# Kernel tuning notes

Measured on AMD Instinct MI355X. Metric: run time of the kernel, lower is better.

## Reference

```python
import jax, jax.numpy as jnp
import numpy as np

B, S, D, H = 2, 2048, 1024, 16
DK = D // H  # 64


def setup_inputs() -> dict:
    key = jax.random.key(0)
    ks = jax.random.split(key, 4)
    scale = 1.0 / np.sqrt(D)
    return {
        "q_input": jax.random.normal(ks[0], (B, S, D), dtype=jnp.float32),
        "W_q": jax.random.normal(ks[1], (D, D), dtype=jnp.float32) * scale,
        "b_q": jnp.zeros((D,), dtype=jnp.float32),
        "W_k": jax.random.normal(ks[2], (D, D), dtype=jnp.float32) * scale,
        "b_k": jnp.zeros((D,), dtype=jnp.float32),
        "W_v": jax.random.normal(ks[3], (D, D), dtype=jnp.float32) * scale,
        "b_v": jnp.zeros((D,), dtype=jnp.float32),
    }


def reference(q_input, W_q, b_q, W_k, b_k, W_v, b_v):
    # Self-attention: k_input and v_input default to q_input in the torch module.
    # nn.Linear computes x @ W.T + b
    q = q_input @ W_q.T + b_q
    k = q_input @ W_k.T + b_k
    v = q_input @ W_v.T + b_v

    # [B,S,D] -> [B,H,S,DK]
    def split_heads(x):
        return x.reshape(B, S, H, DK).transpose(0, 2, 1, 3)

    qh, kh, vh = split_heads(q), split_heads(k), split_heads(v)

    # scores [B,H,S,S]; causal mask added BEFORE scaling (as in source; -inf invariant)
    scores = jnp.einsum("bhqd,bhkd->bhqk", qh, kh)
    causal = jnp.tril(jnp.ones((S, S), dtype=bool))
    scores = jnp.where(causal[None, None], scores, -jnp.inf)
    scores = scores / jnp.sqrt(jnp.float32(DK))
    probs = jax.nn.softmax(scores, axis=-1)
    z = jnp.einsum("bhqk,bhkd->bhqd", probs, vh)  # [B,H,S,DK]
    # [B,H,S,DK] -> [B,S,H,DK] -> [B,S,D]
    return z.transpose(0, 2, 1, 3).reshape(B, S, D)
```

## Files before the change

### kernel.cpp

```cpp
#include <hip/hip_runtime.h>
#include <hip/hip_bf16.h>
#include <stdint.h>

typedef __attribute__((ext_vector_type(8))) short short8;
typedef __attribute__((ext_vector_type(4))) short short4v;
typedef __attribute__((ext_vector_type(4))) float f32x4;

#define B_ 2
#define S_ 2048
#define D_ 1024
#define H_ 16
#define DK_ 64
#define M_ (B_*S_)

#define WS_QKV   0
#define WS_XB    12582912
#define WS_WB    16777216

#define QSCALE (0.125f * 1.44269504088896f)

#define GLL16(g, l) __builtin_amdgcn_global_load_lds( \
    (const __attribute__((address_space(1))) void*)(g), \
    (__attribute__((address_space(3))) void*)(l), 16, 0, 0)

#define WAIT_VM0 asm volatile("s_waitcnt vmcnt(0)" ::: "memory")
#define WAIT_VM4 asm volatile("s_waitcnt vmcnt(4)" ::: "memory")
#define BARRIER_RAW asm volatile("s_barrier" ::: "memory")

static __device__ __forceinline__ short f2bf(float f){
  union { float f; unsigned u; } x; x.f = f;
  unsigned r = x.u + 0x7fff + ((x.u >> 16) & 1);
  return (short)(r >> 16);
}

__global__ __launch_bounds__(256) void cvt_bf16(
    const float* __restrict__ X,  const float* __restrict__ Wq,
    const float* __restrict__ Wk, const float* __restrict__ Wv,
    short* __restrict__ ws)
{
  const int z = blockIdx.z;
  const float* src; short* dst; int n;
  if (z == 0)      { src = X;  dst = ws + WS_XB;               n = M_*D_; }
  else if (z == 1) { src = Wq; dst = ws + WS_WB;               n = D_*D_; }
  else if (z == 2) { src = Wk; dst = ws + WS_WB + D_*D_;       n = D_*D_; }
  else             { src = Wv; dst = ws + WS_WB + 2*(D_*D_);   n = D_*D_; }
  const int stride = gridDim.x * blockDim.x * 4;
  for (int i = (blockIdx.x * blockDim.x + threadIdx.x) * 4; i < n; i += stride) {
    float4 v = *(const float4*)(src + i);
    short4v o;
    o.x = f2bf(v.x); o.y = f2bf(v.y); o.z = f2bf(v.z); o.w = f2bf(v.w);
    *(short4v*)(dst + i) = o;
  }
}

__global__ __launch_bounds__(256, 3) void qkv_gemm(
    const short* __restrict__ ws_in,
    const float* __restrict__ bq, const float* __restrict__ bk,
    const float* __restrict__ bv, short* __restrict__ qkv)
{
  const int z = blockIdx.z;
  const short* X  = ws_in + WS_XB;
  const short* Wm = ws_in + WS_WB + (size_t)z * (D_*D_);
  const float* bias = (z==0) ? bq : (z==1) ? bk : bv;
  short* out = qkv + (size_t)z * (M_*D_);

  __shared__ short lds[24576];

  const int t = threadIdx.x;
  const int w = t >> 6, lane = t & 63;
  const int quad = lane >> 4, l16 = lane & 15;
  const int wm = w & 1, wn = w >> 1;
  const int m0 = blockIdx.y * 128, n0 = blockIdx.x * 128;

  const int lr = lane >> 2, lc = lane & 3;
  const int csrc = lc ^ (lr & 3);
  const size_t arow0 = (size_t)(m0 + w*16     + lr) * D_ + csrc*8;
  const size_t arow1 = (size_t)(m0 + (w+4)*16 + lr) * D_ + csrc*8;
  const size_t brow0 = (size_t)(n0 + w*16     + lr) * D_ + csrc*8;
  const size_t brow1 = (size_t)(n0 + (w+4)*16 + lr) * D_ + csrc*8;

  f32x4 acc[4][4];
  #pragma unroll
  for (int i=0;i<4;i++)
    #pragma unroll
    for (int j=0;j<4;j++) acc[i][j] = (f32x4){0.f,0.f,0.f,0.f};

  #pragma unroll
  for (int p=0;p<2;p++){
    GLL16(X  + arow0 + p*32, lds + p*4096 + (w*16)*32);
    GLL16(X  + arow1 + p*32, lds + p*4096 + ((w+4)*16)*32);
    GLL16(Wm + brow0 + p*32, lds + 12288 + p*4096 + (w*16)*32);
    GLL16(Wm + brow1 + p*32, lds + 12288 + p*4096 + ((w+4)*16)*32);
  }

  const int ca = quad ^ (l16 & 3);
  int cur = 0;
  for (int kk = 0; kk < 32; kk++) {
    if (kk < 31) { WAIT_VM4; }
    else         { WAIT_VM0; }
    BARRIER_RAW;
    if (kk < 30) {
      int slot = cur + 2; if (slot >= 3) slot -= 3;
      const int ko = (kk+2)*32;
      short* An = lds + slot*4096;
      short* Bn = lds + 12288 + slot*4096;
      GLL16(X  + arow0 + ko, An + (w*16)*32);
      GLL16(X  + arow1 + ko, An + ((w+4)*16)*32);
      GLL16(Wm + brow0 + ko, Bn + (w*16)*32);
      GLL16(Wm + brow1 + ko, Bn + ((w+4)*16)*32);
    }
    const short* Ac = lds + cur*4096;
    const short* Bc = lds + 12288 + cur*4096;
    short8 af[4], bfr[4];
    #pragma unroll
    for (int mt=0;mt<4;mt++)
      af[mt] = *(const short8*)(Ac + (wm*64 + mt*16 + l16)*32 + ca*8);
    #pragma unroll
    for (int nt=0;nt<4;nt++)
      bfr[nt] = *(const short8*)(Bc + (wn*64 + nt*16 + l16)*32 + ca*8);
    if (z != 2) {
      #pragma unroll
      for (int mt=0;mt<4;mt++)
        #pragma unroll
        for (int nt=0;nt<4;nt++)
          acc[mt][nt] = __builtin_amdgcn_mfma_f32_16x16x32_bf16(af[mt], bfr[nt], acc[mt][nt], 0,0,0);
    } else {
      #pragma unroll
      for (int nt=0;nt<4;nt++)
        #pragma unroll
        for (int mt=0;mt<4;mt++)
          acc[nt][mt] = __builtin_amdgcn_mfma_f32_16x16x32_bf16(bfr[nt], af[mt], acc[nt][mt], 0,0,0);
    }
    cur = (cur==2) ? 0 : cur+1;
  }

  __syncthreads();

  if (z != 2) {
    const float scale = (z==0) ? QSCALE : 1.0f;
    #pragma unroll
    for (int nt=0;nt<4;nt++){
      const int col_l = wn*64 + nt*16 + l16;
      const float bvv = bias[n0 + col_l];
      #pragma unroll
      for (int mt=0;mt<4;mt++)
        #pragma unroll
        for (int i=0;i<4;i++){
          const int row_l = wm*64 + mt*16 + quad*4 + i;
          lds[row_l*136 + col_l] = f2bf((acc[mt][nt][i] + bvv) * scale);
        }
    }
    __syncthreads();
    #pragma unroll
    for (int k=0;k<8;k++){
      const int cid = k*256 + t;
      const int row = cid >> 4, cc = cid & 15;
      short8 vv = *(const short8*)(lds + row*136 + cc*8);
      const int m = m0 + row, bidx = m >> 11, s = m & 2047;
      const int n = n0 + cc*8, h = n >> 6, dd = n & 63;
      *(short8*)(out + (((size_t)(bidx*H_ + h))*S_ + s)*DK_ + dd) = vv;
    }
  } else {
    #pragma unroll
    for (int nt=0;nt<4;nt++)
      #pragma unroll
      for (int i=0;i<4;i++){
        const int n_l = wn*64 + nt*16 + quad*4 + i;
        const float bvv = bias[n0 + n_l];
        #pragma unroll
        for (int mt=0;mt<4;mt++){
          const int m_l = wm*64 + mt*16 + l16;
          lds[n_l*136 + m_l] = f2bf(acc[nt][mt][i] + bvv);
        }
      }
    __syncthreads();
    #pragma unroll
    for (int k=0;k<8;k++){
      const int cid = k*256 + t;
      const int rowN = cid >> 4, cc = cid & 15;
      short8 vv = *(const short8*)(lds + rowN*136 + cc*8);
      const int n = n0 + rowN, h = n >> 6, dd = n & 63;
      const int m = m0 + cc*8, bidx = m >> 11, s0 = m & 2047;
      *(short8*)(out + (((size_t)(bidx*H_ + h))*DK_ + dd)*S_ + s0) = vv;
    }
  }
}

__global__ __launch_bounds__(256, 3) void attn(
    const short* __restrict__ qkv, float* __restrict__ out)
{
  const int bh = blockIdx.y;
  const int qt = (gridDim.x - 1) - blockIdx.x;
  const short* Q  = qkv + (size_t)bh * (S_*DK_);
  const short* K  = Q + (size_t)(M_*D_);
  const short* VT = qkv + (size_t)(2*M_*D_) + (size_t)bh * (DK_*S_);

  __shared__ short Kbuf[2][4096];
  __shared__ short Vbuf[2][4096];
  __shared__ short Ps[8192];

  const int t = threadIdx.x;
  const int w = t >> 6, lane = t & 63;
  const int quad = lane >> 4, l16 = lane & 15;
  const int sw = l16 & 7;
  const int lr = lane >> 3, lc = lane & 7;
  const int csrc = lc ^ lr;

  short8 bq[2][2];
  #pragma unroll
  for (int kc=0;kc<2;kc++)
    #pragma unroll
    for (int mt=0;mt<2;mt++)
      bq[kc][mt] = *(const short8*)(Q + (size_t)(qt*128 + w*32 + mt*16 + l16)*DK_
                                      + (kc*4 + quad)*8);

  const int nkt = 2*qt + 2;
  #pragma unroll
  for (int j=0;j<2;j++){
    const int rb = (j*4 + w)*8;
    GLL16(K  + (size_t)(rb + lr)*DK_ + csrc*8, &Kbuf[0][0] + rb*64);
    GLL16(VT + (size_t)(rb + lr)*S_  + csrc*8, &Vbuf[0][0] + rb*64);
  }

  f32x4 o[2][4];
  float lsum[2];
  #pragma unroll
  for (int mt=0;mt<2;mt++){
    #pragma unroll
    for (int nd=0;nd<4;nd++) o[mt][nd] = (f32x4){0.f,0.f,0.f,0.f};
    lsum[mt] = 0.f;
  }

  const int pw_half = (quad & 1) * 4;
  const int pw_ckb  = quad >> 1;
  int cur = 0;

  for (int kt = 0; kt < nkt; kt++){
    WAIT_VM0;
    BARRIER_RAW;
    const int nxt = cur ^ 1;
    if (kt + 1 < nkt) {
      const int kb2 = (kt+1)*64;
      short* Kn = &Kbuf[nxt][0];
      short* Vn = &Vbuf[nxt][0];
      #pragma unroll
      for (int j=0;j<2;j++){
        const int rb = (j*4 + w)*8;
        GLL16(K  + (size_t)(kb2 + rb + lr)*DK_ + csrc*8, Kn + rb*64);
        GLL16(VT + (size_t)(rb + lr)*S_ + kb2 + csrc*8,  Vn + rb*64);
      }
    }
    const short* Kc = &Kbuf[cur][0];
    const short* Vc = &Vbuf[cur][0];
    const int kb = kt*64;

    f32x4 sc[4][2];
    #pragma unroll
    for (int ntk=0;ntk<4;ntk++)
      #pragma unroll
      for (int mt=0;mt<2;mt++) sc[ntk][mt] = (f32x4){0.f,0.f,0.f,0.f};
    #pragma unroll
    for (int kc=0;kc<2;kc++){
      const int xch = (kc*4 + quad) ^ sw;
      short8 ak[4];
      #pragma unroll
      for (int ntk=0;ntk<4;ntk++)
        ak[ntk] = *(const short8*)(Kc + (ntk*16 + l16)*64 + xch*8);
      #pragma unroll
      for (int ntk=0;ntk<4;ntk++)
        #pragma unroll
        for (int mt=0;mt<2;mt++)
          sc[ntk][mt] = __builtin_amdgcn_mfma_f32_16x16x32_bf16(ak[ntk], bq[kc][mt], sc[ntk][mt], 0,0,0);
    }

    const int q0w = qt*128 + w*32;
    if (kb + 63 > q0w) {
      #pragma unroll
      for (int ntk=0;ntk<4;ntk++)
        #pragma unroll
        for (int mt=0;mt<2;mt++){
          const int qg = q0w + mt*16 + l16;
          #pragma unroll
          for (int i=0;i<4;i++){
            const int kg = kb + ntk*16 + quad*4 + i;
            if (kg > qg) sc[ntk][mt][i] = -3.0e38f;
          }
        }
    }

    #pragma unroll
    for (int mt=0;mt<2;mt++){
      const int r = w*32 + mt*16 + l16;
      #pragma unroll
      for (int ntk=0;ntk<4;ntk++){
        float p0 = __builtin_amdgcn_exp2f(sc[ntk][mt][0]);
        float p1 = __builtin_amdgcn_exp2f(sc[ntk][mt][1]);
        float p2 = __builtin_amdgcn_exp2f(sc[ntk][mt][2]);
        float p3 = __builtin_amdgcn_exp2f(sc[ntk][mt][3]);
        lsum[mt] += (p0+p1) + (p2+p3);
        unsigned lo = __builtin_amdgcn_perm(__float_as_uint(p1), __float_as_uint(p0), 0x07060302u);
        unsigned hi = __builtin_amdgcn_perm(__float_as_uint(p3), __float_as_uint(p2), 0x07060302u);
        const int slot = (ntk*2 + pw_ckb) ^ sw;
        *(uint2*)(Ps + r*64 + slot*8 + pw_half) = make_uint2(lo, hi);
      }
    }
    asm volatile("" ::: "memory");

    #pragma unroll
    for (int kc=0;kc<2;kc++){
      const int xch = (kc*4 + quad) ^ sw;
      short8 pa[2], vb[4];
      #pragma unroll
      for (int mt=0;mt<2;mt++)
        pa[mt] = *(const short8*)(Ps + (w*32 + mt*16 + l16)*64 + xch*8);
      #pragma unroll
      for (int nd=0;nd<4;nd++)
        vb[nd] = *(const short8*)(Vc + (nd*16 + l16)*64 + xch*8);
      #pragma unroll
      for (int mt=0;mt<2;mt++)
        #pragma unroll
        for (int nd=0;nd<4;nd++)
          o[mt][nd] = __builtin_amdgcn_mfma_f32_16x16x32_bf16(pa[mt], vb[nd], o[mt][nd], 0,0,0);
    }
    cur = nxt;
  }

  const int bb = bh >> 4, h = bh & 15;
  float linv[2];
  #pragma unroll
  for (int mt=0;mt<2;mt++){
    float rs = lsum[mt];
    rs += __shfl_xor(rs, 16, 64);
    rs += __shfl_xor(rs, 32, 64);
    linv[mt] = 1.0f / rs;
  }
  #pragma unroll
  for (int mt=0;mt<2;mt++){
    #pragma unroll
    for (int i=0;i<4;i++){
      const float lw = __shfl(linv[mt], (quad<<4) + (quad<<2) + i, 64);
      const int q = qt*128 + w*32 + mt*16 + quad*4 + i;
      #pragma unroll
      for (int nd=0;nd<4;nd++){
        const int d = nd*16 + l16;
        out[ ((size_t)bb*S_ + q)*D_ + h*DK_ + d ] = o[mt][nd][i] * lw;
      }
    }
  }
}

extern "C" void kernel_launch(void* const* d_in, const int* in_sizes, int n_in,
                              void* d_out, int out_size, void* d_ws, size_t ws_size,
                              hipStream_t stream)
{
  (void)in_sizes; (void)n_in; (void)out_size; (void)ws_size;
  const float* X  = (const float*)d_in[0];
  const float* Wq = (const float*)d_in[1];
  const float* bq = (const float*)d_in[2];
  const float* Wk = (const float*)d_in[3];
  const float* bk = (const float*)d_in[4];
  const float* Wv = (const float*)d_in[5];
  const float* bv = (const float*)d_in[6];
  short* ws  = (short*)d_ws;
  float* out = (float*)d_out;

  dim3 g0(1024, 1, 4);
  cvt_bf16<<<g0, dim3(256,1,1), 0, stream>>>(X, Wq, Wk, Wv, ws);
  dim3 g1(D_/128, M_/128, 3);
  qkv_gemm<<<g1, dim3(256,1,1), 0, stream>>>(ws, bq, bk, bv, ws + WS_QKV);
  dim3 g2(S_/128, B_*H_);
  attn<<<g2, dim3(256,1,1), 0, stream>>>(ws + WS_QKV, out);
}
```

Measured before the change: 181.6 us.

## Replace triple-buffered K=32 GEMM pipeline with single-buffer K=64 tiles

The QKV projection GEMM drops its three-stage LDS ring (K=32 slices, loads issued two steps ahead) and uses one LDS buffer holding a 64-wide K tile. Each step loads the tile, waits for all loads, and runs two MFMA sub-steps under an 8-way XOR swizzle. This halves the number of barrier/wait rounds and cuts LDS use, which may allow more resident blocks. In exchange, global loads no longer overlap with MFMA work inside a block, so latency hiding now depends on occupancy.

Result: slower. 217.9 us (+20.0%).

```diff
diff --git a/kernel.cpp b/kernel.cpp
--- a/kernel.cpp
+++ b/kernel.cpp
@@ -24,7 +24,6 @@
     (__attribute__((address_space(3))) void*)(l), 16, 0, 0)
 
 #define WAIT_VM0 asm volatile("s_waitcnt vmcnt(0)" ::: "memory")
-#define WAIT_VM4 asm volatile("s_waitcnt vmcnt(4)" ::: "memory")
 #define BARRIER_RAW asm volatile("s_barrier" ::: "memory")
 
 static __device__ __forceinline__ short f2bf(float f){
@@ -64,20 +63,17 @@
   const float* bias = (z==0) ? bq : (z==1) ? bk : bv;
   short* out = qkv + (size_t)z * (M_*D_);
 
-  __shared__ short lds[24576];
+  __shared__ short lds[17408];
 
   const int t = threadIdx.x;
   const int w = t >> 6, lane = t & 63;
   const int quad = lane >> 4, l16 = lane & 15;
+  const int sw = l16 & 7;
   const int wm = w & 1, wn = w >> 1;
   const int m0 = blockIdx.y * 128, n0 = blockIdx.x * 128;
 
-  const int lr = lane >> 2, lc = lane & 3;
-  const int csrc = lc ^ (lr & 3);
-  const size_t arow0 = (size_t)(m0 + w*16     + lr) * D_ + csrc*8;
-  const size_t arow1 = (size_t)(m0 + (w+4)*16 + lr) * D_ + csrc*8;
-  const size_t brow0 = (size_t)(n0 + w*16     + lr) * D_ + csrc*8;
-  const size_t brow1 = (size_t)(n0 + (w+4)*16 + lr) * D_ + csrc*8;
+  const int lr = lane >> 3, lc = lane & 7;
+  const int csrc = lc ^ lr;
 
   f32x4 acc[4][4];
   #pragma unroll
@@ -85,53 +81,41 @@
     #pragma unroll
     for (int j=0;j<4;j++) acc[i][j] = (f32x4){0.f,0.f,0.f,0.f};
 
-  #pragma unroll
-  for (int p=0;p<2;p++){
-    GLL16(X  + arow0 + p*32, lds + p*4096 + (w*16)*32);
-    GLL16(X  + arow1 + p*32, lds + p*4096 + ((w+4)*16)*32);
-    GLL16(Wm + brow0 + p*32, lds + 12288 + p*4096 + (w*16)*32);
-    GLL16(Wm + brow1 + p*32, lds + 12288 + p*4096 + ((w+4)*16)*32);
-  }
-
-  const int ca = quad ^ (l16 & 3);
-  int cur = 0;
-  for (int kk = 0; kk < 32; kk++) {
-    if (kk < 31) { WAIT_VM4; }
-    else         { WAIT_VM0; }
+  for (int k0 = 0; k0 < D_; k0 += 64) {
+    #pragma unroll
+    for (int p=0;p<4;p++){
+      const int rb = (p*4 + w)*8;
+      GLL16(X  + (size_t)(m0+rb+lr)*D_ + k0 + csrc*8, lds + rb*64);
+      GLL16(Wm + (size_t)(n0+rb+lr)*D_ + k0 + csrc*8, lds + 8192 + rb*64);
+    }
+    WAIT_VM0;
     BARRIER_RAW;
-    if (kk < 30) {
-      int slot = cur + 2; if (slot >= 3) slot -= 3;
-      const int ko = (kk+2)*32;
-      short* An = lds + slot*4096;
-      short* Bn = lds + 12288 + slot*4096;
-      GLL16(X  + arow0 + ko, An + (w*16)*32);
-      GLL16(X  + arow1 + ko, An + ((w+4)*16)*32);
-      GLL16(Wm + brow0 + ko, Bn + (w*16)*32);
-      GLL16(Wm + brow1 + ko, Bn + ((w+4)*16)*32);
-    }
-    const short* Ac = lds + cur*4096;
-    const short* Bc = lds + 12288 + cur*4096;
-    short8 af[4], bfr[4];
-    #pragma unroll
-    for (int mt=0;mt<4;mt++)
-      af[mt] = *(const short8*)(Ac + (wm*64 + mt*16 + l16)*32 + ca*8);
-    #pragma unroll
-    for (int nt=0;nt<4;nt++)
-      bfr[nt] = *(const short8*)(Bc + (wn*64 + nt*16 + l16)*32 + ca*8);
-    if (z != 2) {
+
+    #pragma unroll
+    for (int kc=0;kc<2;kc++){
+      const int xch = (kc*4 + quad) ^ sw;
+      short8 af[4], bfr[4];
       #pragma unroll
       for (int mt=0;mt<4;mt++)
+        af[mt] = *(const short8*)(lds + (wm*64 + mt*16 + l16)*64 + xch*8);
+      #pragma unroll
+      for (int nt=0;nt<4;nt++)
+        bfr[nt] = *(const short8*)(lds + 8192 + (wn*64 + nt*16 + l16)*64 + xch*8);
+      if (z != 2) {
+        #pragma unroll
+        for (int mt=0;mt<4;mt++)
+          #pragma unroll
+          for (int nt=0;nt<4;nt++)
+            acc[mt][nt] = __builtin_amdgcn_mfma_f32_16x16x32_bf16(af[mt], bfr[nt], acc[mt][nt], 0,0,0);
+      } else {
         #pragma unroll
         for (int nt=0;nt<4;nt++)
-          acc[mt][nt] = __builtin_amdgcn_mfma_f32_16x16x32_bf16(af[mt], bfr[nt], acc[mt][nt], 0,0,0);
-    } else {
-      #pragma unroll
-      for (int nt=0;nt<4;nt++)
-        #pragma unroll
-        for (int mt=0;mt<4;mt++)
-          acc[nt][mt] = __builtin_amdgcn_mfma_f32_16x16x32_bf16(bfr[nt], af[mt], acc[nt][mt], 0,0,0);
-    }
-    cur = (cur==2) ? 0 : cur+1;
+          #pragma unroll
+          for (int mt=0;mt<4;mt++)
+            acc[nt][mt] = __builtin_amdgcn_mfma_f32_16x16x32_bf16(bfr[nt], af[mt], acc[nt][mt], 0,0,0);
+      }
+    }
+    BARRIER_RAW;
   }
 
   __syncthreads();
```
